# Performance work log

Measured on AMD Instinct MI355X. Metric: run time of the kernel, lower is better.

The kernel has to match this reference:

```python
import jax, jax.numpy as jnp
import numpy as np

N_NODES = 100000
N_EDGES = 1600000


def _leaky_relu(x, slope=0.1):
    return jnp.where(x > 0, x, slope * x)


def _sage_conv(x, src, dst, Wl, Wr, b, n_nodes):
    # mean aggregation of source messages onto target nodes (PyG SAGEConv, aggr='mean')
    msg = x[src]                                              # [E, d] gather
    agg_sum = jax.ops.segment_sum(msg, dst, num_segments=n_nodes)
    cnt = jax.ops.segment_sum(jnp.ones((src.shape[0],), x.dtype), dst, num_segments=n_nodes)
    agg = agg_sum / jnp.maximum(cnt, 1.0)[:, None]            # empty neighborhoods -> 0
    # out = lin_l(agg) + lin_r(x); bias lives in lin_l
    return agg @ Wl + x @ Wr + b


def setup_inputs() -> dict:
    key = jax.random.key(0)
    ks = jax.random.split(key, 8)
    x = jax.random.normal(ks[0], (N_NODES, 128), dtype=jnp.float32)
    edge_index = jax.random.randint(ks[1], (2, N_EDGES), 0, N_NODES, dtype=jnp.int32)
    scale = 0.05
    Wl_stack = jax.random.normal(ks[2], (3, 128, 128), dtype=jnp.float32) * scale
    Wr_stack = jax.random.normal(ks[3], (3, 128, 128), dtype=jnp.float32) * scale
    b_stack = jax.random.normal(ks[4], (3, 128), dtype=jnp.float32) * scale
    Wl_out = jax.random.normal(ks[5], (128, 64), dtype=jnp.float32) * scale
    Wr_out = jax.random.normal(ks[6], (128, 64), dtype=jnp.float32) * scale
    b_out = jax.random.normal(ks[7], (64,), dtype=jnp.float32) * scale
    return {"x": x, "edge_index": edge_index, "Wl_stack": Wl_stack,
            "Wr_stack": Wr_stack, "b_stack": b_stack,
            "Wl_out": Wl_out, "Wr_out": Wr_out, "b_out": b_out}


def reference(x, edge_index, Wl_stack, Wr_stack, b_stack, Wl_out, Wr_out, b_out):
    src, dst = edge_index[0], edge_index[1]
    n = x.shape[0]
    h = x
    # conv1 + hidden convs, each followed by LeakyReLU(0.1)
    for i in range(Wl_stack.shape[0]):
        h = _leaky_relu(_sage_conv(h, src, dst, Wl_stack[i], Wr_stack[i], b_stack[i], n))
    # final SAGEConv without activation
    out = _sage_conv(h, src, dst, Wl_out, Wr_out, b_out, n)
    return out
```

## Files before the change

### kernel.cpp

```cpp
#include <hip/hip_runtime.h>

#define NN 100000
#define NNP 100096
#define NE 1600000
#define NBK 391
#define CAP 4608
#define SCCH 4096
#define NSC ((NE + SCCH - 1) / SCCH)
#define MMG 782

typedef __attribute__((ext_vector_type(8))) short bf16x8;
typedef __attribute__((ext_vector_type(4))) float f32x4;

__device__ __forceinline__ float bf2f(unsigned short u) {
    unsigned int v = ((unsigned int)u) << 16;
    return __builtin_bit_cast(float, v);
}
__device__ __forceinline__ unsigned short f2bf(float f) {
    unsigned int u = __builtin_bit_cast(unsigned int, f);
    u += 0x7FFFu + ((u >> 16) & 1u);
    return (unsigned short)(u >> 16);
}
__device__ __forceinline__ unsigned int pk2(float lo, float hi) {
    return (unsigned int)f2bf(lo) | ((unsigned int)f2bf(hi) << 16);
}
__device__ __forceinline__ float bflo(unsigned int v) {
    return __builtin_bit_cast(float, v << 16);
}
__device__ __forceinline__ float bfhi(unsigned int v) {
    return __builtin_bit_cast(float, v & 0xFFFF0000u);
}

__device__ __forceinline__ int mm_gmap(int bid, int off) {
    int x = (bid + off) & 7;
    int j = bid >> 3;
    int g = j;
#pragma unroll
    for (int u = 0; u < 8; ++u)
        if (u < x) g += ((((u - off) & 7) < 6) ? 98 : 97);
    return g;
}


__global__ __launch_bounds__(256) void k_prep(const float* __restrict__ Wl_stack,
                                              const float* __restrict__ Wr_stack,
                                              const float* __restrict__ Wl_out,
                                              const float* __restrict__ Wr_out,
                                              unsigned short* __restrict__ WT,
                                              int* __restrict__ bcur) {
    int i = blockIdx.x * 256 + threadIdx.x;
    const int L3OFF = 3 * 256 * 128;
    const int TOT = L3OFF + 128 * 128;
    if (i < TOT) {
        float v;
        if (i < L3OFF) {
            int l = i / (256 * 128);
            int r = i % (256 * 128);
            int c = r / 128;
            int k = r % 128;
            v = (c < 128) ? Wl_stack[(size_t)(l * 128 + k) * 128 + c]
                          : Wr_stack[(size_t)(l * 128 + k) * 128 + (c - 128)];
        } else {
            int r = i - L3OFF;
            int c = r / 128;
            int k = r % 128;
            v = (c < 64) ? Wl_out[(size_t)k * 64 + c]
                         : Wr_out[(size_t)k * 64 + (c - 64)];
        }
        WT[i] = f2bf(v);
    } else if (i - TOT < NBK) {
        bcur[i - TOT] = (i - TOT) * CAP;
    }
}


__device__ __forceinline__ void scatter_body(int bid, int tid,
                                             const int* __restrict__ src,
                                             const int* __restrict__ dst,
                                             int* __restrict__ bcur,
                                             unsigned int* __restrict__ ebuf,
                                             unsigned char* smem) {
    int* lh = (int*)smem;
    int* lbase = lh + NBK;
    for (int i = tid; i < NBK; i += 256) lh[i] = 0;
    __syncthreads();
    int base = bid * SCCH;
    int lim = min(SCCH, NE - base);
    for (int i = tid; i < lim; i += 256)
        atomicAdd(&lh[dst[base + i] >> 8], 1);
    __syncthreads();
    for (int i = tid; i < NBK; i += 256)
        lbase[i] = lh[i] ? atomicAdd(&bcur[i], lh[i]) : 0;
    __syncthreads();
    for (int i = tid; i < NBK; i += 256) lh[i] = 0;
    __syncthreads();
    for (int i = tid; i < lim; i += 256) {
        int d = dst[base + i];
        int s = src[base + i];
        int b = d >> 8;
        int off = atomicAdd(&lh[b], 1);
        ebuf[(size_t)lbase[b] + off] = ((unsigned)s << 8) | (unsigned)(d & 255);
    }
}

template <int NOUT, bool F32IN>
__device__ __forceinline__ void mm_body(int bid, int xoff, int tid,
                                        const void* __restrict__ Ain,
                                        const unsigned short* __restrict__ WT,
                                        unsigned short* __restrict__ Y,
                                        unsigned short* __restrict__ Z,
                                        unsigned char* lds) {
    constexpr int HALVES = NOUT / 64;
    int wave = tid >> 6, l = tid & 63;
    int lrow = l & 15, g = l >> 4;
    int half, rowblk;
    if (HALVES == 2) {
        int gm = mm_gmap(bid, xoff);
        half = gm & 1;
        rowblk = gm >> 1;
    } else {
        half = 0;
        rowblk = bid;
    }
    int rbase = rowblk * 256 + wave * 64;

    {
        const unsigned char* wsrc = (const unsigned char*)(WT + (size_t)half * 128 * 128);
#pragma unroll
        for (int j = 0; j < 8; ++j) {
            int lin = (j * 256 + tid) * 16;
            uint4 v = *(const uint4*)(wsrc + lin);
            int row = lin >> 8;
            int colb = lin & 255;
            *(uint4*)(lds + row * 256 + (colb ^ ((row & 7) << 4))) = v;
        }
    }

    bf16x8 af[4][4];
#pragma unroll
    for (int s = 0; s < 4; ++s) {
        int row = rbase + s * 16 + lrow;
#pragma unroll
        for (int ks = 0; ks < 4; ++ks) {
            if (F32IN) {
                int rc = row < NN ? row : NN - 1;
                const float* ap = (const float*)Ain + (size_t)rc * 128 + ks * 32 + g * 8;
                float4 a = *(const float4*)ap;
                float4 b = *(const float4*)(ap + 4);
                uint4 u;
                u.x = pk2(a.x, a.y); u.y = pk2(a.z, a.w);
                u.z = pk2(b.x, b.y); u.w = pk2(b.z, b.w);
                af[s][ks] = __builtin_bit_cast(bf16x8, u);
            } else {
                af[s][ks] = *(const bf16x8*)((const unsigned short*)Ain
                                             + (size_t)row * 128 + ks * 32 + g * 8);
            }
        }
    }
    __syncthreads();

#pragma unroll
    for (int cg = 0; cg < 8; ++cg) {
        int c0 = cg * 16;
        int rl = c0 + lrow;
        bf16x8 bfr[4];
#pragma unroll
        for (int ks = 0; ks < 4; ++ks) {
            int colb = ks * 64 + g * 16;
            bfr[ks] = *(const bf16x8*)(lds + rl * 256 + (colb ^ ((rl & 7) << 4)));
        }
        int gc0 = half * 128 + c0;
        unsigned short* dstp = (gc0 < NOUT) ? Y : Z;
        int cb = ((gc0 < NOUT) ? gc0 : gc0 - NOUT) + g * 4;
#pragma unroll
        for (int s = 0; s < 4; ++s) {
            f32x4 acc = {0.f, 0.f, 0.f, 0.f};
#pragma unroll
            for (int ks = 0; ks < 4; ++ks)
                acc = __builtin_amdgcn_mfma_f32_16x16x32_bf16(bfr[ks], af[s][ks], acc, 0, 0, 0);
            int row = rbase + s * 16 + lrow;
            uint2 w;
            w.x = pk2(acc[0], acc[1]);
            w.y = pk2(acc[2], acc[3]);
            *(uint2*)(dstp + (size_t)row * NOUT + cb) = w;
        }
    }
}


__global__ __launch_bounds__(256) void k_fused0(const int* __restrict__ src,
                                                const int* __restrict__ dst,
                                                int* __restrict__ bcur,
                                                unsigned int* __restrict__ ebuf,
                                                const float* __restrict__ x,
                                                const unsigned short* __restrict__ WT,
                                                unsigned short* __restrict__ Y,
                                                unsigned short* __restrict__ Z) {
    __shared__ unsigned char smem[32768];
    int tid = threadIdx.x;
    if (blockIdx.x < NSC) {
        scatter_body(blockIdx.x, tid, src, dst, bcur, ebuf, smem);
    } else {
        mm_body<128, true>(blockIdx.x - NSC, 7, tid, x, WT, Y, Z, smem);
    }
}


template <int NOUT>
__global__ __launch_bounds__(256) void k_mm(const unsigned short* __restrict__ Ain,
                                            const unsigned short* __restrict__ WT,
                                            unsigned short* __restrict__ Y,
                                            unsigned short* __restrict__ Z) {
    __shared__ unsigned char lds[32768];
    mm_body<NOUT, false>(blockIdx.x, 0, threadIdx.x, Ain, WT, Y, Z, lds);
}


__global__ __launch_bounds__(256) void kb_csr(const unsigned int* __restrict__ ebuf,
                                              const int* __restrict__ bcur,
                                              int* __restrict__ row_beg,
                                              int* __restrict__ row_end,
                                              int* __restrict__ csr) {
    __shared__ int sdeg[256], spre[256];
    int bkt = blockIdx.x;
    int tid = threadIdx.x;
    int nbase = bkt << 8;
    int ebeg = bkt * CAP;
    int eend = bcur[bkt];
    sdeg[tid] = 0;
    __syncthreads();
    for (int e = ebeg + tid; e < eend; e += 256)
        atomicAdd(&sdeg[ebuf[e] & 255], 1);
    __syncthreads();
    spre[tid] = sdeg[tid];
    __syncthreads();
#pragma unroll
    for (int off = 1; off < 256; off <<= 1) {
        int t = (tid >= off) ? spre[tid - off] : 0;
        __syncthreads();
        if (tid >= off) spre[tid] += t;
        __syncthreads();
    }
    int excl = spre[tid] - sdeg[tid];
    if (nbase + tid < NN) {
        row_beg[nbase + tid] = ebeg + excl;
        row_end[nbase + tid] = ebeg + excl + sdeg[tid];
    }
    __syncthreads();
    sdeg[tid] = excl;
    __syncthreads();
    for (int e = ebeg + tid; e < eend; e += 256) {
        unsigned int v = ebuf[e];
        int p = atomicAdd(&sdeg[v & 255], 1);
        csr[ebeg + p] = (int)(v >> 8);
    }
}


template <int NOUT, bool RELU>
__global__ __launch_bounds__(256) void k_aggb(const unsigned short* __restrict__ Y,
                                              const unsigned short* __restrict__ Z,
                                              const int* __restrict__ row_beg,
                                              const int* __restrict__ row_end,
                                              const int* __restrict__ csr,
                                              const float* __restrict__ b,
                                              unsigned short* __restrict__ outb,
                                              float* __restrict__ outf) {
    int lane = threadIdx.x & 63;
    int n = __builtin_amdgcn_readfirstlane(blockIdx.x * 4 + (threadIdx.x >> 6));
    if (n >= NN) return;
    int beg = __builtin_amdgcn_readfirstlane(row_beg[n]);
    int end = __builtin_amdgcn_readfirstlane(row_end[n]);
    float inv = (end > beg) ? 1.0f / (float)(end - beg) : 0.0f;

    if (NOUT == 128) {
        const int lane2 = lane * 2;
        float a0 = 0.f, a1 = 0.f;
        int e = beg;
        for (; e + 8 <= end; e += 8) {
            int s0 = csr[e + 0], s1 = csr[e + 1], s2 = csr[e + 2], s3 = csr[e + 3];
            int s4 = csr[e + 4], s5 = csr[e + 5], s6 = csr[e + 6], s7 = csr[e + 7];
            unsigned int v0 = *(const unsigned int*)(Y + (size_t)s0 * 128 + lane2);
            unsigned int v1 = *(const unsigned int*)(Y + (size_t)s1 * 128 + lane2);
            unsigned int v2 = *(const unsigned int*)(Y + (size_t)s2 * 128 + lane2);
            unsigned int v3 = *(const unsigned int*)(Y + (size_t)s3 * 128 + lane2);
            unsigned int v4 = *(const unsigned int*)(Y + (size_t)s4 * 128 + lane2);
            unsigned int v5 = *(const unsigned int*)(Y + (size_t)s5 * 128 + lane2);
            unsigned int v6 = *(const unsigned int*)(Y + (size_t)s6 * 128 + lane2);
            unsigned int v7 = *(const unsigned int*)(Y + (size_t)s7 * 128 + lane2);
            a0 += bflo(v0) + bflo(v1) + bflo(v2) + bflo(v3)
                + bflo(v4) + bflo(v5) + bflo(v6) + bflo(v7);
            a1 += bfhi(v0) + bfhi(v1) + bfhi(v2) + bfhi(v3)
                + bfhi(v4) + bfhi(v5) + bfhi(v6) + bfhi(v7);
        }
        for (; e + 4 <= end; e += 4) {
            int s0 = csr[e + 0], s1 = csr[e + 1], s2 = csr[e + 2], s3 = csr[e + 3];
            unsigned int v0 = *(const unsigned int*)(Y + (size_t)s0 * 128 + lane2);
            unsigned int v1 = *(const unsigned int*)(Y + (size_t)s1 * 128 + lane2);
            unsigned int v2 = *(const unsigned int*)(Y + (size_t)s2 * 128 + lane2);
            unsigned int v3 = *(const unsigned int*)(Y + (size_t)s3 * 128 + lane2);
            a0 += bflo(v0) + bflo(v1) + bflo(v2) + bflo(v3);
            a1 += bfhi(v0) + bfhi(v1) + bfhi(v2) + bfhi(v3);
        }
        for (; e < end; ++e) {
            int s = csr[e];
            unsigned int v = *(const unsigned int*)(Y + (size_t)s * 128 + lane2);
            a0 += bflo(v);
            a1 += bfhi(v);
        }
        unsigned int zv = *(const unsigned int*)(Z + (size_t)n * 128 + lane2);
        float2 bb = *(const float2*)(b + lane2);
        float o0 = a0 * inv + bflo(zv) + bb.x;
        float o1 = a1 * inv + bfhi(zv) + bb.y;
        if (RELU) {
            o0 = o0 > 0.f ? o0 : 0.1f * o0;
            o1 = o1 > 0.f ? o1 : 0.1f * o1;
        }
        *(unsigned int*)(outb + (size_t)n * 128 + lane2) = pk2(o0, o1);
    } else {
        float a0 = 0.f;
        int e = beg;
        for (; e + 8 <= end; e += 8) {
            int s0 = csr[e + 0], s1 = csr[e + 1], s2 = csr[e + 2], s3 = csr[e + 3];
            int s4 = csr[e + 4], s5 = csr[e + 5], s6 = csr[e + 6], s7 = csr[e + 7];
            float f0 = bf2f(Y[(size_t)s0 * 64 + lane]);
            float f1 = bf2f(Y[(size_t)s1 * 64 + lane]);
            float f2 = bf2f(Y[(size_t)s2 * 64 + lane]);
            float f3 = bf2f(Y[(size_t)s3 * 64 + lane]);
            float f4 = bf2f(Y[(size_t)s4 * 64 + lane]);
            float f5 = bf2f(Y[(size_t)s5 * 64 + lane]);
            float f6 = bf2f(Y[(size_t)s6 * 64 + lane]);
            float f7 = bf2f(Y[(size_t)s7 * 64 + lane]);
            a0 += f0 + f1 + f2 + f3 + f4 + f5 + f6 + f7;
        }
        for (; e + 4 <= end; e += 4) {
            int s0 = csr[e + 0], s1 = csr[e + 1], s2 = csr[e + 2], s3 = csr[e + 3];
            float f0 = bf2f(Y[(size_t)s0 * 64 + lane]);
            float f1 = bf2f(Y[(size_t)s1 * 64 + lane]);
            float f2 = bf2f(Y[(size_t)s2 * 64 + lane]);
            float f3 = bf2f(Y[(size_t)s3 * 64 + lane]);
            a0 += f0 + f1 + f2 + f3;
        }
        for (; e < end; ++e) {
            int s = csr[e];
            a0 += bf2f(Y[(size_t)s * 64 + lane]);
        }
        float o = a0 * inv + bf2f(Z[(size_t)n * 64 + lane]) + b[lane];
        if (RELU) o = o > 0.f ? o : 0.1f * o;
        outf[(size_t)n * 64 + lane] = o;
    }
}


extern "C" void kernel_launch(void* const* d_in, const int* in_sizes, int n_in,
                              void* d_out, int out_size, void* d_ws, size_t ws_size,
                              hipStream_t stream) {
    const float* x        = (const float*)d_in[0];
    const int*   ei       = (const int*)d_in[1];
    const float* Wl_stack = (const float*)d_in[2];
    const float* Wr_stack = (const float*)d_in[3];
    const float* b_stack  = (const float*)d_in[4];
    const float* Wl_out   = (const float*)d_in[5];
    const float* Wr_out   = (const float*)d_in[6];
    const float* b_out    = (const float*)d_in[7];
    float* out = (float*)d_out;

    unsigned short* hb = (unsigned short*)d_ws;
    unsigned short* Yb = hb + (size_t)NNP * 128;
    unsigned short* Zb = Yb + (size_t)NNP * 128;
    unsigned short* WT = Zb + (size_t)NNP * 128;
    unsigned int* ebuf = (unsigned int*)(WT + 114688);
    int* csr     = (int*)(ebuf + (size_t)NBK * CAP);
    int* row_beg = csr + (size_t)NBK * CAP;
    int* row_end = row_beg + NN;
    int* bcur    = row_end + NN;

    const int* src = ei;
    const int* dst = ei + NE;

    k_prep<<<450, 256, 0, stream>>>(Wl_stack, Wr_stack, Wl_out, Wr_out, WT, bcur);

    k_fused0<<<NSC + MMG, 256, 0, stream>>>(src, dst, bcur, ebuf, x, WT, Yb, Zb);

    kb_csr<<<NBK, 256, 0, stream>>>(ebuf, bcur, row_beg, row_end, csr);
    k_aggb<128, true><<<(NN + 3) / 4, 256, 0, stream>>>(Yb, Zb, row_beg, row_end, csr,
                                                        b_stack, hb, nullptr);
    for (int l = 1; l < 3; ++l) {
        k_mm<128><<<MMG, 256, 0, stream>>>(hb, WT + l * 32768, Yb, Zb);
        k_aggb<128, true><<<(NN + 3) / 4, 256, 0, stream>>>(Yb, Zb, row_beg, row_end, csr,
                                                            b_stack + l * 128, hb, nullptr);
    }
    k_mm<64><<<NNP / 256, 256, 0, stream>>>(hb, WT + 98304, Yb, Zb);
    k_aggb<64, false><<<(NN + 3) / 4, 256, 0, stream>>>(Yb, Zb, row_beg, row_end, csr,
                                                        b_out, nullptr, out);
}
```

Measured before the change: 358.2 us.

## Fuse mean aggregation with next layer's matmul via LDS-staged hidden tile

```diff
diff --git a/kernel.cpp b/kernel.cpp
--- a/kernel.cpp
+++ b/kernel.cpp
@@ -8,6 +8,7 @@
 #define SCCH 4096
 #define NSC ((NE + SCCH - 1) / SCCH)
 #define MMG 782
+#define FAGGB 1563
 
 typedef __attribute__((ext_vector_type(8))) short bf16x8;
 typedef __attribute__((ext_vector_type(4))) float f32x4;
@@ -103,25 +104,17 @@
     }
 }
 
-template <int NOUT, bool F32IN>
-__device__ __forceinline__ void mm_body(int bid, int xoff, int tid,
-                                        const void* __restrict__ Ain,
-                                        const unsigned short* __restrict__ WT,
-                                        unsigned short* __restrict__ Y,
-                                        unsigned short* __restrict__ Z,
-                                        unsigned char* lds) {
-    constexpr int HALVES = NOUT / 64;
+__device__ __forceinline__ void mm0_body(int bid, int xoff, int tid,
+                                         const float* __restrict__ Ain,
+                                         const unsigned short* __restrict__ WT,
+                                         unsigned short* __restrict__ Y,
+                                         unsigned short* __restrict__ Z,
+                                         unsigned char* lds) {
     int wave = tid >> 6, l = tid & 63;
     int lrow = l & 15, g = l >> 4;
-    int half, rowblk;
-    if (HALVES == 2) {
-        int gm = mm_gmap(bid, xoff);
-        half = gm & 1;
-        rowblk = gm >> 1;
-    } else {
-        half = 0;
-        rowblk = bid;
-    }
+    int gm = mm_gmap(bid, xoff);
+    int half = gm & 1;
+    int rowblk = gm >> 1;
     int rbase = rowblk * 256 + wave * 64;
 
     {
@@ -140,21 +133,16 @@
 #pragma unroll
     for (int s = 0; s < 4; ++s) {
         int row = rbase + s * 16 + lrow;
+        int rc = row < NN ? row : NN - 1;
 #pragma unroll
         for (int ks = 0; ks < 4; ++ks) {
-            if (F32IN) {
-                int rc = row < NN ? row : NN - 1;
-                const float* ap = (const float*)Ain + (size_t)rc * 128 + ks * 32 + g * 8;
-                float4 a = *(const float4*)ap;
-                float4 b = *(const float4*)(ap + 4);
-                uint4 u;
-                u.x = pk2(a.x, a.y); u.y = pk2(a.z, a.w);
-                u.z = pk2(b.x, b.y); u.w = pk2(b.z, b.w);
-                af[s][ks] = __builtin_bit_cast(bf16x8, u);
-            } else {
-                af[s][ks] = *(const bf16x8*)((const unsigned short*)Ain
-                                             + (size_t)row * 128 + ks * 32 + g * 8);
-            }
+            const float* ap = Ain + (size_t)rc * 128 + ks * 32 + g * 8;
+            float4 a = *(const float4*)ap;
+            float4 b = *(const float4*)(ap + 4);
+            uint4 u;
+            u.x = pk2(a.x, a.y); u.y = pk2(a.z, a.w);
+            u.z = pk2(b.x, b.y); u.w = pk2(b.z, b.w);
+            af[s][ks] = __builtin_bit_cast(bf16x8, u);
         }
     }
     __syncthreads();
@@ -170,8 +158,8 @@
             bfr[ks] = *(const bf16x8*)(lds + rl * 256 + (colb ^ ((rl & 7) << 4)));
         }
         int gc0 = half * 128 + c0;
-        unsigned short* dstp = (gc0 < NOUT) ? Y : Z;
-        int cb = ((gc0 < NOUT) ? gc0 : gc0 - NOUT) + g * 4;
+        unsigned short* dstp = (gc0 < 128) ? Y : Z;
+        int cb = ((gc0 < 128) ? gc0 : gc0 - 128) + g * 4;
 #pragma unroll
         for (int s = 0; s < 4; ++s) {
             f32x4 acc = {0.f, 0.f, 0.f, 0.f};
@@ -182,7 +170,7 @@
             uint2 w;
             w.x = pk2(acc[0], acc[1]);
             w.y = pk2(acc[2], acc[3]);
-            *(uint2*)(dstp + (size_t)row * NOUT + cb) = w;
+            *(uint2*)(dstp + (size_t)row * 128 + cb) = w;
         }
     }
 }
@@ -201,18 +189,8 @@
     if (blockIdx.x < NSC) {
         scatter_body(blockIdx.x, tid, src, dst, bcur, ebuf, smem);
     } else {
-        mm_body<128, true>(blockIdx.x - NSC, 7, tid, x, WT, Y, Z, smem);
-    }
-}
-
-
-template <int NOUT>
-__global__ __launch_bounds__(256) void k_mm(const unsigned short* __restrict__ Ain,
-                                            const unsigned short* __restrict__ WT,
-                                            unsigned short* __restrict__ Y,
-                                            unsigned short* __restrict__ Z) {
-    __shared__ unsigned char lds[32768];
-    mm_body<NOUT, false>(blockIdx.x, 0, threadIdx.x, Ain, WT, Y, Z, lds);
+        mm0_body(blockIdx.x - NSC, 7, tid, x, WT, Y, Z, smem);
+    }
 }
 
 
@@ -257,15 +235,121 @@
 }
 
 
-template <int NOUT, bool RELU>
-__global__ __launch_bounds__(256) void k_aggb(const unsigned short* __restrict__ Y,
+template <int NOUTN>
+__global__ __launch_bounds__(256) void k_fagg(const unsigned short* __restrict__ Y,
                                               const unsigned short* __restrict__ Z,
                                               const int* __restrict__ row_beg,
                                               const int* __restrict__ row_end,
                                               const int* __restrict__ csr,
                                               const float* __restrict__ b,
-                                              unsigned short* __restrict__ outb,
-                                              float* __restrict__ outf) {
+                                              const unsigned short* __restrict__ WTn,
+                                              unsigned short* __restrict__ Yn,
+                                              unsigned short* __restrict__ Zn) {
+    constexpr int N2 = 2 * NOUTN;
+    constexpr int CGB = N2 / 64;
+    __shared__ unsigned char hlds[64 * 256];
+
+    int tid = threadIdx.x;
+    int wave = tid >> 6, lane = tid & 63;
+    int lrow = lane & 15, g = lane >> 4;
+    int nodebase = blockIdx.x * 64;
+    const int lane2 = lane * 2;
+
+    for (int r = 0; r < 16; ++r) {
+        int rl = wave * 16 + r;
+        int n = __builtin_amdgcn_readfirstlane(nodebase + rl);
+        float o0 = 0.f, o1 = 0.f;
+        if (n < NN) {
+            int beg = __builtin_amdgcn_readfirstlane(row_beg[n]);
+            int end = __builtin_amdgcn_readfirstlane(row_end[n]);
+            float inv = (end > beg) ? 1.0f / (float)(end - beg) : 0.0f;
+            float a0 = 0.f, a1 = 0.f;
+            int e = beg;
+            for (; e + 8 <= end; e += 8) {
+                int s0 = csr[e + 0], s1 = csr[e + 1], s2 = csr[e + 2], s3 = csr[e + 3];
+                int s4 = csr[e + 4], s5 = csr[e + 5], s6 = csr[e + 6], s7 = csr[e + 7];
+                unsigned int v0 = *(const unsigned int*)(Y + (size_t)s0 * 128 + lane2);
+                unsigned int v1 = *(const unsigned int*)(Y + (size_t)s1 * 128 + lane2);
+                unsigned int v2 = *(const unsigned int*)(Y + (size_t)s2 * 128 + lane2);
+                unsigned int v3 = *(const unsigned int*)(Y + (size_t)s3 * 128 + lane2);
+                unsigned int v4 = *(const unsigned int*)(Y + (size_t)s4 * 128 + lane2);
+                unsigned int v5 = *(const unsigned int*)(Y + (size_t)s5 * 128 + lane2);
+                unsigned int v6 = *(const unsigned int*)(Y + (size_t)s6 * 128 + lane2);
+                unsigned int v7 = *(const unsigned int*)(Y + (size_t)s7 * 128 + lane2);
+                a0 += bflo(v0) + bflo(v1) + bflo(v2) + bflo(v3)
+                    + bflo(v4) + bflo(v5) + bflo(v6) + bflo(v7);
+                a1 += bfhi(v0) + bfhi(v1) + bfhi(v2) + bfhi(v3)
+                    + bfhi(v4) + bfhi(v5) + bfhi(v6) + bfhi(v7);
+            }
+            for (; e + 4 <= end; e += 4) {
+                int s0 = csr[e + 0], s1 = csr[e + 1], s2 = csr[e + 2], s3 = csr[e + 3];
+                unsigned int v0 = *(const unsigned int*)(Y + (size_t)s0 * 128 + lane2);
+                unsigned int v1 = *(const unsigned int*)(Y + (size_t)s1 * 128 + lane2);
+                unsigned int v2 = *(const unsigned int*)(Y + (size_t)s2 * 128 + lane2);
+                unsigned int v3 = *(const unsigned int*)(Y + (size_t)s3 * 128 + lane2);
+                a0 += bflo(v0) + bflo(v1) + bflo(v2) + bflo(v3);
+                a1 += bfhi(v0) + bfhi(v1) + bfhi(v2) + bfhi(v3);
+            }
+            for (; e < end; ++e) {
+                int s = csr[e];
+                unsigned int v = *(const unsigned int*)(Y + (size_t)s * 128 + lane2);
+                a0 += bflo(v);
+                a1 += bfhi(v);
+            }
+            unsigned int zv = *(const unsigned int*)(Z + (size_t)n * 128 + lane2);
+            float2 bb = *(const float2*)(b + lane2);
+            o0 = a0 * inv + bflo(zv) + bb.x;
+            o1 = a1 * inv + bfhi(zv) + bb.y;
+            o0 = o0 > 0.f ? o0 : 0.1f * o0;
+            o1 = o1 > 0.f ? o1 : 0.1f * o1;
+        }
+        *(unsigned int*)(hlds + rl * 256 + ((lane * 4) ^ ((rl & 7) << 4))) = pk2(o0, o1);
+    }
+    __syncthreads();
+
+    bf16x8 af[4][4];
+#pragma unroll
+    for (int s = 0; s < 4; ++s) {
+        int row = s * 16 + lrow;
+#pragma unroll
+        for (int ks = 0; ks < 4; ++ks) {
+            int colb = ks * 64 + g * 16;
+            af[s][ks] = *(const bf16x8*)(hlds + row * 256 + (colb ^ ((row & 7) << 4)));
+        }
+    }
+    int cbase = wave * (N2 / 4);
+#pragma unroll
+    for (int cg = 0; cg < CGB; ++cg) {
+        int c0 = cbase + cg * 16;
+        bf16x8 bfr[4];
+#pragma unroll
+        for (int ks = 0; ks < 4; ++ks)
+            bfr[ks] = *(const bf16x8*)(WTn + (size_t)(c0 + lrow) * 128 + ks * 32 + g * 8);
+        unsigned short* dstp = (c0 < NOUTN) ? Yn : Zn;
+        int cb = ((c0 < NOUTN) ? c0 : c0 - NOUTN) + g * 4;
+#pragma unroll
+        for (int s = 0; s < 4; ++s) {
+            f32x4 acc = {0.f, 0.f, 0.f, 0.f};
+#pragma unroll
+            for (int ks = 0; ks < 4; ++ks)
+                acc = __builtin_amdgcn_mfma_f32_16x16x32_bf16(bfr[ks], af[s][ks], acc, 0, 0, 0);
+            int row = nodebase + s * 16 + lrow;
+            uint2 w;
+            w.x = pk2(acc[0], acc[1]);
+            w.y = pk2(acc[2], acc[3]);
+            *(uint2*)(dstp + (size_t)row * NOUTN + cb) = w;
+        }
+    }
+}
+
+
+__global__ __launch_bounds__(256) void k_agg_out(const unsigned short* __restrict__ Y,
+                                                 const unsigned short* __restrict__ Z,
+                                                 const int* __restrict__ row_beg,
+                                                 const int* __restrict__ row_end,
+                                                 const int* __restrict__ csr,
+                                                 const float* __restrict__ b,
+                                                 float* __restrict__ outf) {
     int lane = threadIdx.x & 63;
     int n = __builtin_amdgcn_readfirstlane(blockIdx.x * 4 + (threadIdx.x >> 6));
     if (n >= NN) return;
@@ -273,82 +357,35 @@
     int end = __builtin_amdgcn_readfirstlane(row_end[n]);
     float inv = (end > beg) ? 1.0f / (float)(end - beg) : 0.0f;
 
-    if (NOUT == 128) {
-        const int lane2 = lane * 2;
-        float a0 = 0.f, a1 = 0.f;
-        int e = beg;
-        for (; e + 8 <= end; e += 8) {
-            int s0 = csr[e + 0], s1 = csr[e + 1], s2 = csr[e + 2], s3 = csr[e + 3];
-            int s4 = csr[e + 4], s5 = csr[e + 5], s6 = csr[e + 6], s7 = csr[e + 7];
-            unsigned int v0 = *(const unsigned int*)(Y + (size_t)s0 * 128 + lane2);
-            unsigned int v1 = *(const unsigned int*)(Y + (size_t)s1 * 128 + lane2);
-            unsigned int v2 = *(const unsigned int*)(Y + (size_t)s2 * 128 + lane2);
-            unsigned int v3 = *(const unsigned int*)(Y + (size_t)s3 * 128 + lane2);
-            unsigned int v4 = *(const unsigned int*)(Y + (size_t)s4 * 128 + lane2);
-            unsigned int v5 = *(const unsigned int*)(Y + (size_t)s5 * 128 + lane2);
-            unsigned int v6 = *(const unsigned int*)(Y + (size_t)s6 * 128 + lane2);
-            unsigned int v7 = *(const unsigned int*)(Y + (size_t)s7 * 128 + lane2);
-            a0 += bflo(v0) + bflo(v1) + bflo(v2) + bflo(v3)
-                + bflo(v4) + bflo(v5) + bflo(v6) + bflo(v7);
-            a1 += bfhi(v0) + bfhi(v1) + bfhi(v2) + bfhi(v3)
-                + bfhi(v4) + bfhi(v5) + bfhi(v6) + bfhi(v7);
-        }
-        for (; e + 4 <= end; e += 4) {
-            int s0 = csr[e + 0], s1 = csr[e + 1], s2 = csr[e + 2], s3 = csr[e + 3];
-            unsigned int v0 = *(const unsigned int*)(Y + (size_t)s0 * 128 + lane2);
-            unsigned int v1 = *(const unsigned int*)(Y + (size_t)s1 * 128 + lane2);
-            unsigned int v2 = *(const unsigned int*)(Y + (size_t)s2 * 128 + lane2);
-            unsigned int v3 = *(const unsigned int*)(Y + (size_t)s3 * 128 + lane2);
-            a0 += bflo(v0) + bflo(v1) + bflo(v2) + bflo(v3);
-            a1 += bfhi(v0) + bfhi(v1) + bfhi(v2) + bfhi(v3);
-        }
-        for (; e < end; ++e) {
-            int s = csr[e];
-            unsigned int v = *(const unsigned int*)(Y + (size_t)s * 128 + lane2);
-            a0 += bflo(v);
-            a1 += bfhi(v);
-        }
-        unsigned int zv = *(const unsigned int*)(Z + (size_t)n * 128 + lane2);
-        float2 bb = *(const float2*)(b + lane2);
-        float o0 = a0 * inv + bflo(zv) + bb.x;
-        float o1 = a1 * inv + bfhi(zv) + bb.y;
-        if (RELU) {
-            o0 = o0 > 0.f ? o0 : 0.1f * o0;
-            o1 = o1 > 0.f ? o1 : 0.1f * o1;
-        }
-        *(unsigned int*)(outb + (size_t)n * 128 + lane2) = pk2(o0, o1);
-    } else {
-        float a0 = 0.f;
-        int e = beg;
-        for (; e + 8 <= end; e += 8) {
-            int s0 = csr[e + 0], s1 = csr[e + 1], s2 = csr[e + 2], s3 = csr[e + 3];
-            int s4 = csr[e + 4], s5 = csr[e + 5], s6 = csr[e + 6], s7 = csr[e + 7];
-            float f0 = bf2f(Y[(size_t)s0 * 64 + lane]);
-            float f1 = bf2f(Y[(size_t)s1 * 64 + lane]);
-            float f2 = bf2f(Y[(size_t)s2 * 64 + lane]);
-            float f3 = bf2f(Y[(size_t)s3 * 64 + lane]);
-            float f4 = bf2f(Y[(size_t)s4 * 64 + lane]);
-            float f5 = bf2f(Y[(size_t)s5 * 64 + lane]);
-            float f6 = bf2f(Y[(size_t)s6 * 64 + lane]);
-            float f7 = bf2f(Y[(size_t)s7 * 64 + lane]);
-            a0 += f0 + f1 + f2 + f3 + f4 + f5 + f6 + f7;
-        }
-        for (; e + 4 <= end; e += 4) {
-            int s0 = csr[e + 0], s1 = csr[e + 1], s2 = csr[e + 2], s3 = csr[e + 3];
-            float f0 = bf2f(Y[(size_t)s0 * 64 + lane]);
-            float f1 = bf2f(Y[(size_t)s1 * 64 + lane]);
-            float f2 = bf2f(Y[(size_t)s2 * 64 + lane]);
-            float f3 = bf2f(Y[(size_t)s3 * 64 + lane]);
-            a0 += f0 + f1 + f2 + f3;
-        }
-        for (; e < end; ++e) {
-            int s = csr[e];
-            a0 += bf2f(Y[(size_t)s * 64 + lane]);
-        }
-        float o = a0 * inv + bf2f(Z[(size_t)n * 64 + lane]) + b[lane];
-        if (RELU) o = o > 0.f ? o : 0.1f * o;
-        outf[(size_t)n * 64 + lane] = o;
-    }
+    float a0 = 0.f;
+    int e = beg;
+    for (; e + 8 <= end; e += 8) {
+        int s0 = csr[e + 0], s1 = csr[e + 1], s2 = csr[e + 2], s3 = csr[e + 3];
+        int s4 = csr[e + 4], s5 = csr[e + 5], s6 = csr[e + 6], s7 = csr[e + 7];
+        float f0 = bf2f(Y[(size_t)s0 * 64 + lane]);
+        float f1 = bf2f(Y[(size_t)s1 * 64 + lane]);
+        float f2 = bf2f(Y[(size_t)s2 * 64 + lane]);
+        float f3 = bf2f(Y[(size_t)s3 * 64 + lane]);
+        float f4 = bf2f(Y[(size_t)s4 * 64 + lane]);
+        float f5 = bf2f(Y[(size_t)s5 * 64 + lane]);
+        float f6 = bf2f(Y[(size_t)s6 * 64 + lane]);
+        float f7 = bf2f(Y[(size_t)s7 * 64 + lane]);
+        a0 += f0 + f1 + f2 + f3 + f4 + f5 + f6 + f7;
+    }
+    for (; e + 4 <= end; e += 4) {
+        int s0 = csr[e + 0], s1 = csr[e + 1], s2 = csr[e + 2], s3 = csr[e + 3];
+        float f0 = bf2f(Y[(size_t)s0 * 64 + lane]);
+        float f1 = bf2f(Y[(size_t)s1 * 64 + lane]);
+        float f2 = bf2f(Y[(size_t)s2 * 64 + lane]);
+        float f3 = bf2f(Y[(size_t)s3 * 64 + lane]);
+        a0 += f0 + f1 + f2 + f3;
+    }
+    for (; e < end; ++e) {
+        int s = csr[e];
+        a0 += bf2f(Y[(size_t)s * 64 + lane]);
+    }
+    float o = a0 * inv + bf2f(Z[(size_t)n * 64 + lane]) + b[lane];
+    outf[(size_t)n * 64 + lane] = o;
 }
 
 
@@ -365,10 +402,11 @@
     const float* b_out    = (const float*)d_in[7];
     float* out = (float*)d_out;
 
-    unsigned short* hb = (unsigned short*)d_ws;
-    unsigned short* Yb = hb + (size_t)NNP * 128;
-    unsigned short* Zb = Yb + (size_t)NNP * 128;
-    unsigned short* WT = Zb + (size_t)NNP * 128;
+    unsigned short* Y0 = (unsigned short*)d_ws;
+    unsigned short* Z0 = Y0 + (size_t)NNP * 128;
+    unsigned short* Y1 = Z0 + (size_t)NNP * 128;
+    unsigned short* Z1 = Y1 + (size_t)NNP * 128;
+    unsigned short* WT = Z1 + (size_t)NNP * 128;
     unsigned int* ebuf = (unsigned int*)(WT + 114688);
     int* csr     = (int*)(ebuf + (size_t)NBK * CAP);
     int* row_beg = csr + (size_t)NBK * CAP;
@@ -380,17 +418,17 @@
 
     k_prep<<<450, 256, 0, stream>>>(Wl_stack, Wr_stack, Wl_out, Wr_out, WT, bcur);
 
-    k_fused0<<<NSC + MMG, 256, 0, stream>>>(src, dst, bcur, ebuf, x, WT, Yb, Zb);
+    k_fused0<<<NSC + MMG, 256, 0, stream>>>(src, dst, bcur, ebuf, x, WT, Y0, Z0);
 
     kb_csr<<<NBK, 256, 0, stream>>>(ebuf, bcur, row_beg, row_end, csr);
-    k_aggb<128, true><<<(NN + 3) / 4, 256, 0, stream>>>(Yb, Zb, row_beg, row_end, csr,
-                                                        b_stack, hb, nullptr);
-    for (int l = 1; l < 3; ++l) {
-        k_mm<128><<<MMG, 256, 0, stream>>>(hb, WT + l * 32768, Yb, Zb);
-        k_aggb<128, true><<<(NN + 3) / 4, 256, 0, stream>>>(Yb, Zb, row_beg, row_end, csr,
-                                                            b_stack + l * 128, hb, nullptr);
-    }
-    k_mm<64><<<NNP / 256, 256, 0, stream>>>(hb, WT + 98304, Yb, Zb);
-    k_aggb<64, false><<<(NN + 3) / 4, 256, 0, stream>>>(Yb, Zb, row_beg, row_end, csr,
-                                                        b_out, nullptr, out);
-}
+
+    k_fagg<128><<<FAGGB, 256, 0, stream>>>(Y0, Z0, row_beg, row_end, csr,
+                                           b_stack, WT + 32768, Y1, Z1);
+    k_fagg<128><<<FAGGB, 256, 0, stream>>>(Y1, Z1, row_beg, row_end, csr,
+                                           b_stack + 128, WT + 65536, Y0, Z0);
+    k_fagg<64><<<FAGGB, 256, 0, stream>>>(Y0, Z0, row_beg, row_end, csr,
+                                          b_stack + 256, WT + 98304, Y1, Z1);
+
+    k_agg_out<<<(NN + 3) / 4, 256, 0, stream>>>(Y1, Z1, row_beg, row_end, csr,
+                                                b_out, out);
+}
```

New measurement: 390.8 us. +9.1%, slower.
